# Kernel tuning notes

Hardware: AMD Instinct MI355X
Metric: run time of the kernel (lower is better)

## Reference

```python
import jax, jax.numpy as jnp
import numpy as np

NEG_INF = -1e30


def setup_inputs() -> dict:
    key = jax.random.key(0)
    k1, k2 = jax.random.split(key)
    x = jax.random.normal(k1, (8, 512, 64, 64), dtype=jnp.float32)
    mask = jax.random.randint(k2, (64, 64), 0, 2, dtype=jnp.int32)  # 1 = masked (hole)
    return {"x": x, "mask": mask}


def reference(x, mask):
    # Shift-Net style random multi-shift (shift_sz=1, stride=1, triple_weight=1).
    # x: [B, C, H, W]; former = decoder half, latter = encoder half.
    B, C, H, W = x.shape
    c2 = C // 2
    HW = H * W
    former = x[:, :c2]
    latter = x[:, c2:]

    flag = mask.reshape(HW) > 0  # True where masked (needs filling)

    # Random neighbor selection: for every spatial position, pick a uniformly
    # random NON-masked source position (argmax of uniform scores with masked
    # sources disabled). Deterministic via fixed key, jit-friendly static shapes.
    rkey = jax.random.key(42)
    scores = jax.random.uniform(rkey, (HW, HW), dtype=jnp.float32)
    scores = jnp.where(flag[None, :], NEG_INF, scores)  # sources must be known region
    nb = jnp.argmax(scores, axis=1)  # [HW] random known-region index per position

    latter_flat = latter.reshape(B, c2, HW)
    gathered = latter_flat[:, :, nb]  # [B, c2, HW] shift-gathered encoder features
    # Paste gathered features only inside the masked region; zeros elsewhere.
    shift = jnp.where(flag[None, None, :], gathered, jnp.zeros_like(gathered))
    shift = shift.reshape(B, c2, H, W)

    return jnp.concatenate([former, latter, shift], axis=1)  # [B, 3C/2, H, W]
```

## Files before the change

kernel.cpp:

```cpp
#include <hip/hip_runtime.h>
#include <stdint.h>

static constexpr int HW = 4096;
static constexpr int CC = 512;
static constexpr int C2 = 256;
static constexpr int OC = 768;

__device__ __forceinline__ uint32_t rotl32(uint32_t x, int d) {
  return (x << d) | (x >> (32 - d));
}

__device__ __forceinline__ void threefry_0_42(uint32_t x0, uint32_t x1,
                                              uint32_t& o0, uint32_t& o1) {
  const uint32_t k0 = 0u;
  const uint32_t k1 = 42u;
  const uint32_t k2 = 0x1BD11BDAu ^ k0 ^ k1;
  x0 += k0; x1 += k1;
#define TF_ROUND(r) { x0 += x1; x1 = rotl32(x1, (r)); x1 ^= x0; }
  TF_ROUND(13) TF_ROUND(15) TF_ROUND(26) TF_ROUND(6)
  x0 += k1; x1 += k2 + 1u;
  TF_ROUND(17) TF_ROUND(29) TF_ROUND(16) TF_ROUND(24)
  x0 += k2; x1 += k0 + 2u;
  TF_ROUND(13) TF_ROUND(15) TF_ROUND(26) TF_ROUND(6)
  x0 += k0; x1 += k1 + 3u;
  TF_ROUND(17) TF_ROUND(29) TF_ROUND(16) TF_ROUND(24)
  x0 += k1; x1 += k2 + 4u;
  TF_ROUND(13) TF_ROUND(15) TF_ROUND(26) TF_ROUND(6)
  x0 += k2; x1 += k0 + 5u;
#undef TF_ROUND
  o0 = x0; o1 = x1;
}

__device__ __forceinline__ uint32_t jax_bits32(uint32_t e) {
  uint32_t o0, o1;
  threefry_0_42(0u, e, o0, o1);
  return o0 ^ o1;
}

__global__ __launch_bounds__(256) void copy_argmax_kernel(
    const float* __restrict__ x, const int* __restrict__ mask,
    int* __restrict__ idx, float* __restrict__ out) {
  const int p = blockIdx.x;
  if ((p & 1) == 0) {
    const int q = p >> 1;
    const int b = q >> 9, ch = q & 511;
    const float4* src = (const float4*)(x + ((size_t)b * CC + ch) * HW);
    float4* dst = (float4*)(out + ((size_t)b * OC + ch) * HW);
#pragma unroll
    for (int r = 0; r < 4; ++r) {
      const int t = threadIdx.x + r * 256;
      dst[t] = src[t];
    }
    return;
  }
  const int i = p >> 1;
  if (mask[i] == 0) {
    if (threadIdx.x == 0) idx[i] = -1;
    return;
  }

  __shared__ int cols[HW];
  __shared__ int chunk_cnt[64];
  __shared__ int chunk_off[64];
  __shared__ int total_sh;
  const int wave = threadIdx.x >> 6;
  const int lane = threadIdx.x & 63;

#pragma unroll
  for (int t = wave; t < 64; t += 4) {
    const int j = t * 64 + lane;
    const unsigned long long bal = __ballot(mask[j] == 0);
    if (lane == 0) chunk_cnt[t] = __popcll(bal);
  }
  __syncthreads();
  if (wave == 0) {
    int v = chunk_cnt[lane];
    int inc = v;
#pragma unroll
    for (int off = 1; off < 64; off <<= 1) {
      const int u = __shfl_up(inc, off);
      if (lane >= off) inc += u;
    }
    chunk_off[lane] = inc - v;
    if (lane == 63) total_sh = inc;
  }
  __syncthreads();
#pragma unroll
  for (int t = wave; t < 64; t += 4) {
    const int j = t * 64 + lane;
    const bool un = (mask[j] == 0);
    const unsigned long long bal = __ballot(un);
    if (un) {
      const int pos = chunk_off[t] + __popcll(bal & ((1ULL << lane) - 1ULL));
      cols[pos] = j;
    }
  }
  __syncthreads();

  const int m = total_sh;
  const uint32_t e0 = (uint32_t)i * 4096u;
  long long best = -1;
  for (int t = threadIdx.x; t < m; t += 256) {
    const int j = cols[t];
    const uint32_t bits = jax_bits32(e0 + (uint32_t)j);
    const long long k = ((long long)(bits >> 9) << 12) | (long long)(4095 - j);
    best = (k > best) ? k : best;
  }
#pragma unroll
  for (int off = 32; off > 0; off >>= 1) {
    const long long a = __shfl_down(best, off);
    best = (a > best) ? a : best;
  }
  __shared__ long long s[4];
  if (lane == 0) s[wave] = best;
  __syncthreads();
  if (threadIdx.x == 0) {
    long long a = s[0];
#pragma unroll
    for (int w = 1; w < 4; ++w) if (s[w] > a) a = s[w];
    idx[i] = (a >= 0) ? (4095 - (int)(a & 0xFFFLL)) : 0;
  }
}

__global__ __launch_bounds__(256) void gather_kernel(const float* __restrict__ x,
                                                     const int* __restrict__ idx,
                                                     float* __restrict__ out) {
  const int p = blockIdx.x;
  const int b = p >> 8, c = p & 255;
  const float* row = x + ((size_t)b * CC + C2 + c) * HW;
  float* oshift = out + ((size_t)b * OC + 512 + c) * HW;
  __shared__ float lds[HW];
  const float4* row4 = (const float4*)row;
  float4* lds4 = (float4*)lds;
#pragma unroll
  for (int r = 0; r < 4; ++r) {
    const int t = threadIdx.x + r * 256;
    lds4[t] = row4[t];
  }
  __syncthreads();
  const int4* idx4 = (const int4*)idx;
  float4* oshift4 = (float4*)oshift;
#pragma unroll
  for (int r = 0; r < 4; ++r) {
    const int t = threadIdx.x + r * 256;
    const int4 nb = idx4[t];
    float4 v;
    v.x = (nb.x >= 0) ? lds[nb.x] : 0.0f;
    v.y = (nb.y >= 0) ? lds[nb.y] : 0.0f;
    v.z = (nb.z >= 0) ? lds[nb.z] : 0.0f;
    v.w = (nb.w >= 0) ? lds[nb.w] : 0.0f;
    oshift4[t] = v;
  }
}

extern "C" void kernel_launch(void* const* d_in, const int* in_sizes, int n_in,
                              void* d_out, int out_size, void* d_ws, size_t ws_size,
                              hipStream_t stream) {
  const float* x  = (const float*)d_in[0];
  const int* mask = (const int*)d_in[1];
  float* out      = (float*)d_out;
  int* idx        = (int*)d_ws;

  copy_argmax_kernel<<<8192, 256, 0, stream>>>(x, mask, idx, out);
  gather_kernel<<<2048, 256, 0, stream>>>(x, idx, out);
}
```

Measured before the change: 162.9 us.

## Batch argmax rows per block and fuse latter copy into gather kernel

The argmax blocks now handle eight rows each, so the compacted list of unmasked columns is built once per block instead of once per masked row. This removes repeated mask scans and prefix sums and cuts the block count from 4096 argmax blocks to 512. The latter-half copy moves into the gather kernel, which already reads that channel row into LDS, so the separate copy no longer reads x a second time. In exchange, each argmax block runs its eight rows serially with extra barriers, and the gather kernel writes two outputs per block.

Result: slower. 176.4 us (+8.3%).

```diff
diff --git a/kernel.cpp b/kernel.cpp
--- a/kernel.cpp
+++ b/kernel.cpp
@@ -5,6 +5,8 @@
 static constexpr int CC = 512;
 static constexpr int C2 = 256;
 static constexpr int OC = 768;
+static constexpr int NIDX_BLOCKS = 512;
+static constexpr int ROWS_PER_BLOCK = 8;
 
 __device__ __forceinline__ uint32_t rotl32(uint32_t x, int d) {
   return (x << d) | (x >> (32 - d));
@@ -37,15 +39,15 @@
   return o0 ^ o1;
 }
 
-__global__ __launch_bounds__(256) void copy_argmax_kernel(
+__global__ __launch_bounds__(256) void former_idx_kernel(
     const float* __restrict__ x, const int* __restrict__ mask,
     int* __restrict__ idx, float* __restrict__ out) {
   const int p = blockIdx.x;
-  if ((p & 1) == 0) {
-    const int q = p >> 1;
-    const int b = q >> 9, ch = q & 511;
-    const float4* src = (const float4*)(x + ((size_t)b * CC + ch) * HW);
-    float4* dst = (float4*)(out + ((size_t)b * OC + ch) * HW);
+  if (p >= NIDX_BLOCKS) {
+    const int q = p - NIDX_BLOCKS;
+    const int b = q >> 8, c = q & 255;
+    const float4* src = (const float4*)(x + ((size_t)b * CC + c) * HW);
+    float4* dst = (float4*)(out + ((size_t)b * OC + c) * HW);
 #pragma unroll
     for (int r = 0; r < 4; ++r) {
       const int t = threadIdx.x + r * 256;
@@ -53,16 +55,12 @@
     }
     return;
   }
-  const int i = p >> 1;
-  if (mask[i] == 0) {
-    if (threadIdx.x == 0) idx[i] = -1;
-    return;
-  }
 
   __shared__ int cols[HW];
   __shared__ int chunk_cnt[64];
   __shared__ int chunk_off[64];
   __shared__ int total_sh;
+  __shared__ long long s[4];
   const int wave = threadIdx.x >> 6;
   const int lane = threadIdx.x & 63;
 
@@ -98,48 +96,57 @@
   __syncthreads();
 
   const int m = total_sh;
-  const uint32_t e0 = (uint32_t)i * 4096u;
-  long long best = -1;
-  for (int t = threadIdx.x; t < m; t += 256) {
-    const int j = cols[t];
-    const uint32_t bits = jax_bits32(e0 + (uint32_t)j);
-    const long long k = ((long long)(bits >> 9) << 12) | (long long)(4095 - j);
-    best = (k > best) ? k : best;
-  }
+  const int row0 = p * ROWS_PER_BLOCK;
+  for (int r = 0; r < ROWS_PER_BLOCK; ++r) {
+    const int i = row0 + r;
+    if (mask[i] == 0) {
+      if (threadIdx.x == 0) idx[i] = -1;
+      continue;
+    }
+    const uint32_t e0 = (uint32_t)i * 4096u;
+    long long best = -1;
+    for (int t = threadIdx.x; t < m; t += 256) {
+      const int j = cols[t];
+      const uint32_t bits = jax_bits32(e0 + (uint32_t)j);
+      const long long k = ((long long)(bits >> 9) << 12) | (long long)(4095 - j);
+      best = (k > best) ? k : best;
+    }
 #pragma unroll
-  for (int off = 32; off > 0; off >>= 1) {
-    const long long a = __shfl_down(best, off);
-    best = (a > best) ? a : best;
-  }
-  __shared__ long long s[4];
-  if (lane == 0) s[wave] = best;
-  __syncthreads();
-  if (threadIdx.x == 0) {
-    long long a = s[0];
+    for (int off = 32; off > 0; off >>= 1) {
+      const long long a = __shfl_down(best, off);
+      best = (a > best) ? a : best;
+    }
+    if (lane == 0) s[wave] = best;
+    __syncthreads();
+    if (threadIdx.x == 0) {
+      long long a = s[0];
 #pragma unroll
-    for (int w = 1; w < 4; ++w) if (s[w] > a) a = s[w];
-    idx[i] = (a >= 0) ? (4095 - (int)(a & 0xFFFLL)) : 0;
+      for (int w = 1; w < 4; ++w) if (s[w] > a) a = s[w];
+      idx[i] = (a >= 0) ? (4095 - (int)(a & 0xFFFLL)) : 0;
+    }
+    __syncthreads();
   }
 }
 
-__global__ __launch_bounds__(256) void gather_kernel(const float* __restrict__ x,
-                                                     const int* __restrict__ idx,
-                                                     float* __restrict__ out) {
+__global__ __launch_bounds__(256) void latter_gather_kernel(
+    const float* __restrict__ x, const int* __restrict__ idx,
+    float* __restrict__ out) {
   const int p = blockIdx.x;
   const int b = p >> 8, c = p & 255;
-  const float* row = x + ((size_t)b * CC + C2 + c) * HW;
-  float* oshift = out + ((size_t)b * OC + 512 + c) * HW;
+  const float4* src4 = (const float4*)(x + ((size_t)b * CC + C2 + c) * HW);
+  float4* lat4 = (float4*)(out + ((size_t)b * OC + C2 + c) * HW);
+  float4* shf4 = (float4*)(out + ((size_t)b * OC + 2 * C2 + c) * HW);
   __shared__ float lds[HW];
-  const float4* row4 = (const float4*)row;
   float4* lds4 = (float4*)lds;
 #pragma unroll
   for (int r = 0; r < 4; ++r) {
     const int t = threadIdx.x + r * 256;
-    lds4[t] = row4[t];
+    const float4 v = src4[t];
+    lds4[t] = v;
+    lat4[t] = v;
   }
   __syncthreads();
   const int4* idx4 = (const int4*)idx;
-  float4* oshift4 = (float4*)oshift;
 #pragma unroll
   for (int r = 0; r < 4; ++r) {
     const int t = threadIdx.x + r * 256;
@@ -149,7 +156,7 @@
     v.y = (nb.y >= 0) ? lds[nb.y] : 0.0f;
     v.z = (nb.z >= 0) ? lds[nb.z] : 0.0f;
     v.w = (nb.w >= 0) ? lds[nb.w] : 0.0f;
-    oshift4[t] = v;
+    shf4[t] = v;
   }
 }
 
@@ -161,6 +168,6 @@
   float* out      = (float*)d_out;
   int* idx        = (int*)d_ws;
 
-  copy_argmax_kernel<<<8192, 256, 0, stream>>>(x, mask, idx, out);
-  gather_kernel<<<2048, 256, 0, stream>>>(x, idx, out);
+  former_idx_kernel<<<NIDX_BLOCKS + 2048, 256, 0, stream>>>(x, mask, idx, out);
+  latter_gather_kernel<<<2048, 256, 0, stream>>>(x, idx, out);
 }
```

## Fuse plane copy and argmax into one block, drop LDS compaction

Applied to the files above, without the earlier changes.

Each block now copies one channel plane and also computes the random-neighbour argmax for spatial row q, which halves the grid from 8192 to 4096 blocks. The argmax no longer compacts unmasked columns into a 16KB LDS list with ballot, scan and three barriers. Instead every thread loops over all columns and skips masked ones with a branch. This is meant to cut block count, shared-memory pressure and barrier cost, and to overlap the memory-bound copy with the hash compute. In exchange, lanes diverge on masked columns, so about half of each wave sits idle during the hash loop.

Result: slower. 174.0 us (+6.8%).

```diff
diff --git a/kernel.cpp b/kernel.cpp
--- a/kernel.cpp
+++ b/kernel.cpp
@@ -40,72 +40,36 @@
 __global__ __launch_bounds__(256) void copy_argmax_kernel(
     const float* __restrict__ x, const int* __restrict__ mask,
     int* __restrict__ idx, float* __restrict__ out) {
-  const int p = blockIdx.x;
-  if ((p & 1) == 0) {
-    const int q = p >> 1;
-    const int b = q >> 9, ch = q & 511;
-    const float4* src = (const float4*)(x + ((size_t)b * CC + ch) * HW);
-    float4* dst = (float4*)(out + ((size_t)b * OC + ch) * HW);
-#pragma unroll
-    for (int r = 0; r < 4; ++r) {
-      const int t = threadIdx.x + r * 256;
-      dst[t] = src[t];
-    }
-    return;
-  }
-  const int i = p >> 1;
+  const int q = blockIdx.x;
+  const int b = q >> 9, ch = q & 511;
+
+  const float4* src = (const float4*)(x + ((size_t)b * CC + ch) * HW);
+  float4* dst = (float4*)(out + ((size_t)b * OC + ch) * HW);
+  const float4 v0 = src[threadIdx.x];
+  const float4 v1 = src[threadIdx.x + 256];
+  const float4 v2 = src[threadIdx.x + 512];
+  const float4 v3 = src[threadIdx.x + 768];
+  dst[threadIdx.x]       = v0;
+  dst[threadIdx.x + 256] = v1;
+  dst[threadIdx.x + 512] = v2;
+  dst[threadIdx.x + 768] = v3;
+
+  const int i = q;
   if (mask[i] == 0) {
     if (threadIdx.x == 0) idx[i] = -1;
     return;
   }
-
-  __shared__ int cols[HW];
-  __shared__ int chunk_cnt[64];
-  __shared__ int chunk_off[64];
-  __shared__ int total_sh;
+  const uint32_t e0 = (uint32_t)i * 4096u;
+  long long best = -1;
+  for (int j = threadIdx.x; j < HW; j += 256) {
+    if (mask[j] == 0) {
+      const uint32_t bits = jax_bits32(e0 + (uint32_t)j);
+      const long long k = ((long long)(bits >> 9) << 12) | (long long)(4095 - j);
+      best = (k > best) ? k : best;
+    }
+  }
   const int wave = threadIdx.x >> 6;
   const int lane = threadIdx.x & 63;
-
-#pragma unroll
-  for (int t = wave; t < 64; t += 4) {
-    const int j = t * 64 + lane;
-    const unsigned long long bal = __ballot(mask[j] == 0);
-    if (lane == 0) chunk_cnt[t] = __popcll(bal);
-  }
-  __syncthreads();
-  if (wave == 0) {
-    int v = chunk_cnt[lane];
-    int inc = v;
-#pragma unroll
-    for (int off = 1; off < 64; off <<= 1) {
-      const int u = __shfl_up(inc, off);
-      if (lane >= off) inc += u;
-    }
-    chunk_off[lane] = inc - v;
-    if (lane == 63) total_sh = inc;
-  }
-  __syncthreads();
-#pragma unroll
-  for (int t = wave; t < 64; t += 4) {
-    const int j = t * 64 + lane;
-    const bool un = (mask[j] == 0);
-    const unsigned long long bal = __ballot(un);
-    if (un) {
-      const int pos = chunk_off[t] + __popcll(bal & ((1ULL << lane) - 1ULL));
-      cols[pos] = j;
-    }
-  }
-  __syncthreads();
-
-  const int m = total_sh;
-  const uint32_t e0 = (uint32_t)i * 4096u;
-  long long best = -1;
-  for (int t = threadIdx.x; t < m; t += 256) {
-    const int j = cols[t];
-    const uint32_t bits = jax_bits32(e0 + (uint32_t)j);
-    const long long k = ((long long)(bits >> 9) << 12) | (long long)(4095 - j);
-    best = (k > best) ? k : best;
-  }
 #pragma unroll
   for (int off = 32; off > 0; off >>= 1) {
     const long long a = __shfl_down(best, off);
@@ -161,6 +125,6 @@
   float* out      = (float*)d_out;
   int* idx        = (int*)d_ws;
 
-  copy_argmax_kernel<<<8192, 256, 0, stream>>>(x, mask, idx, out);
+  copy_argmax_kernel<<<4096, 256, 0, stream>>>(x, mask, idx, out);
   gather_kernel<<<2048, 256, 0, stream>>>(x, idx, out);
 }
```
